# Optimization experiments

Hardware: AMD Instinct MI355X
Metric: run time of the kernel (lower is better)

## Reference

```python
import jax, jax.numpy as jnp
import numpy as np
import math

B = 65536
N_NUM = 64; N_CAT = 16; CAT_SIZE = 1000; EMB = 16
ND = 64; NA = 64; OUT = ND + NA; NSTEPS = 5; GAMMA = 1.5
NFEAT = N_NUM + N_CAT * EMB          # 320
NGROUPS = N_NUM + N_CAT              # 80
GROUP_IDX = np.repeat(np.arange(NGROUPS), [1] * N_NUM + [EMB] * N_CAT)  # len 320
RES_SCALE = math.sqrt(0.5)
BN_EPS = 1e-5


def setup_inputs() -> dict:
    keys = iter(jax.random.split(jax.random.key(0), 64))
    def rn(shape, std):
        return jax.random.normal(next(keys), shape, jnp.float32) * std
    def mk_bn(c, lead=()):
        # stacked (scale, bias, running_mean, running_var) along axis -2
        s = 1.0 + 0.05 * jax.random.normal(next(keys), (*lead, c), jnp.float32)
        b = 0.05 * jax.random.normal(next(keys), (*lead, c), jnp.float32)
        m = 0.05 * jax.random.normal(next(keys), (*lead, c), jnp.float32)
        v = 1.0 + 0.1 * jax.random.uniform(next(keys), (*lead, c), dtype=jnp.float32)
        return jnp.stack([s, b, m, v], axis=-2)
    inp = {}
    inp["x_num"] = jax.random.normal(next(keys), (B, N_NUM), jnp.float32)
    inp["x_cat"] = jax.random.randint(next(keys), (B, N_CAT), 0, CAT_SIZE)
    inp["emb_W"] = rn((N_CAT, CAT_SIZE, EMB), 0.1)
    inp["in_bn"] = mk_bn(NFEAT)
    inp["sh_W0"] = rn((NFEAT, 2 * OUT), 1.0 / math.sqrt(NFEAT))
    inp["sh_b0"] = jnp.zeros((2 * OUT,), jnp.float32)
    inp["sh_bn0"] = mk_bn(2 * OUT)
    inp["sh_W1"] = rn((OUT, 2 * OUT), 1.0 / math.sqrt(OUT))
    inp["sh_b1"] = jnp.zeros((2 * OUT,), jnp.float32)
    inp["sh_bn1"] = mk_bn(2 * OUT)
    inp["init_W"] = rn((2, OUT, 2 * OUT), 1.0 / math.sqrt(OUT))
    inp["init_b"] = jnp.zeros((2, 2 * OUT), jnp.float32)
    inp["init_bn"] = mk_bn(2 * OUT, (2,))
    inp["step_W"] = rn((NSTEPS, 2, OUT, 2 * OUT), 1.0 / math.sqrt(OUT))
    inp["step_b"] = jnp.zeros((NSTEPS, 2, 2 * OUT), jnp.float32)
    inp["step_bn"] = mk_bn(2 * OUT, (NSTEPS, 2))
    inp["att_W"] = rn((NSTEPS, NA, NGROUPS), 1.0 / math.sqrt(NA))
    inp["att_b"] = jnp.zeros((NSTEPS, NGROUPS), jnp.float32)
    inp["att_bn"] = mk_bn(NGROUPS, (NSTEPS,))
    inp["out_W"] = rn((ND, 1), 1.0 / math.sqrt(ND))
    inp["out_b"] = jnp.zeros((1,), jnp.float32)
    return inp


def bn_apply(x, p):
    s, b, m, v = p  # each [C]
    return (x - m) * jax.lax.rsqrt(v + BN_EPS) * s + b


def glu_layer(x, W, b, bn):
    h = bn_apply(x @ W + b, bn)          # [B, 2*OUT]
    o, g = jnp.split(h, 2, axis=1)
    return o * jax.nn.sigmoid(g)


def glu_block(x, W, b, bn):
    y = glu_layer(x, W, b, bn)
    return (x + y) * RES_SCALE if x.shape == y.shape else y


def sparsemax(z):
    # along axis=1; Martins & Astudillo 2016
    zs = -jnp.sort(-z, axis=1)
    cs = jnp.cumsum(zs, axis=1)
    r = jnp.arange(1, z.shape[1] + 1, dtype=z.dtype)
    support = (1.0 + r * zs) > cs
    k = jnp.maximum(support.sum(axis=1, keepdims=True), 1)
    cs_k = jnp.take_along_axis(cs, k - 1, axis=1)
    tau = (cs_k - 1.0) / k.astype(z.dtype)
    return jnp.maximum(z - tau, 0.0)


def _forward(x_num, x_cat, emb_W, in_bn, sh_W0, sh_b0, sh_bn0, sh_W1, sh_b1, sh_bn1,
             init_W, init_b, init_bn, step_W, step_b, step_bn, att_W, att_b, att_bn,
             out_W, out_b):
    # categorical embeddings: [B, N_CAT, EMB] -> [B, N_CAT*EMB]
    emb = emb_W[np.arange(N_CAT)[None, :], x_cat].reshape(x_cat.shape[0], -1)
    x = jnp.concatenate([x_num, emb], axis=1)  # [B, NFEAT]
    x = bn_apply(x, in_bn)

    def ft_shared(h):
        h = glu_block(h, sh_W0, sh_b0, sh_bn0)   # 320 -> 128, no residual
        return glu_block(h, sh_W1, sh_b1, sh_bn1)  # residual

    def ft_indep(h, W, b, bn):
        for i in range(W.shape[0]):
            h = glu_block(h, W[i], b[i], bn[i])
        return h

    out0 = ft_indep(ft_shared(x), init_W, init_b, init_bn)
    a = out0[:, ND:]
    prior = jnp.ones((x.shape[0], NGROUPS), x.dtype)
    decision_sum = jnp.zeros((x.shape[0], ND), x.dtype)
    for step in range(NSTEPS):
        logits = bn_apply(a @ att_W[step] + att_b[step], att_bn[step]) * prior
        mask_group = sparsemax(logits)           # [B, NGROUPS]
        prior = prior * (GAMMA - mask_group)
        mask = mask_group[:, GROUP_IDX]          # [B, NFEAT] (repeat_interleave)
        out = ft_indep(ft_shared(mask * x), step_W[step], step_b[step], step_bn[step])
        d, a = out[:, :ND], out[:, ND:]
        decision_sum = decision_sum + jax.nn.relu(d)
    return decision_sum @ out_W + out_b          # [B, 1]


def reference(x_num, x_cat, emb_W, in_bn, sh_W0, sh_b0, sh_bn0, sh_W1, sh_b1, sh_bn1,
              init_W, init_b, init_bn, step_W, step_b, step_bn, att_W, att_b, att_bn,
              out_W, out_b):
    return _forward(x_num, x_cat, emb_W, in_bn, sh_W0, sh_b0, sh_bn0, sh_W1, sh_b1,
                    sh_bn1, init_W, init_b, init_bn, step_W, step_b, step_bn,
                    att_W, att_b, att_bn, out_W, out_b)
```

## Files before the change

kernel.cpp:

```cpp
#include <hip/hip_runtime.h>
#include <math.h>
#include <stdint.h>

typedef _Float16 half_t;
typedef _Float16 half8 __attribute__((ext_vector_type(8)));
typedef __fp16 fp16x2 __attribute__((ext_vector_type(2)));
typedef float floatx4 __attribute__((ext_vector_type(4)));
typedef float floatx16 __attribute__((ext_vector_type(16)));

constexpr float BN_EPS_C = 1e-5f;
constexpr float RES_SCALE_C = 0.70710678118654752f;
constexpr float GAMMA_C = 1.5f;
#define B_TOT 65536

__device__ __forceinline__ uint32_t pack2(float y) {
    const half_t h = (half_t)y;
    const half_t l = (half_t)(y - (float)h);
    union { half_t f; unsigned short u; } a, b; a.f = h; b.f = l;
    return (uint32_t)a.u | ((uint32_t)b.u << 16);
}
__device__ __forceinline__ void unpack2(uint32_t v, half_t& h, half_t& l) {
    union { unsigned short u; half_t f; } a, b;
    a.u = (unsigned short)(v & 0xffffu); b.u = (unsigned short)(v >> 16);
    h = a.f; l = b.f;
}
__device__ __forceinline__ void split_pair(float y0, float y1, half_t& h0, half_t& l0, half_t& h1, half_t& l1) {
    fp16x2 hh = __builtin_amdgcn_cvt_pkrtz(y0, y1);
    fp16x2 ll = __builtin_amdgcn_cvt_pkrtz(y0 - (float)hh.x, y1 - (float)hh.y);
    h0 = (half_t)hh.x; l0 = (half_t)ll.x; h1 = (half_t)hh.y; l1 = (half_t)ll.y;
}
__device__ __forceinline__ void pack2_pair(float y0, float y1, uint32_t& w0, uint32_t& w1) {
    fp16x2 hh = __builtin_amdgcn_cvt_pkrtz(y0, y1);
    fp16x2 ll = __builtin_amdgcn_cvt_pkrtz(y0 - (float)hh.x, y1 - (float)hh.y);
    const uint32_t hb = __builtin_bit_cast(uint32_t, hh);
    const uint32_t lb = __builtin_bit_cast(uint32_t, ll);
    w0 = (hb & 0xffffu) | (lb << 16);
    w1 = (hb >> 16) | (lb & 0xffff0000u);
}
__device__ __forceinline__ void unpack8(const uint32_t* wv, half8& h, half8& l) {
#pragma unroll
    for (int j = 0; j < 8; ++j) {
        half_t hh, ll; unpack2(wv[j], hh, ll);
        h[j] = hh; l[j] = ll;
    }
}

__global__ void wsplit_kernel(const float* __restrict__ sh_W0, const float* __restrict__ sh_W1,
                              const float* __restrict__ init_W, const float* __restrict__ step_W,
                              half_t* __restrict__ Wh, half_t* __restrict__ Wl)
{
    const int b = blockIdx.x, n = threadIdx.x;
    const float* src; int k; size_t base;
    if (b < 320)      { src = sh_W0;           k = b;       base = 0; }
    else if (b < 448) { src = sh_W1;           k = b - 320; base = 81920; }
    else if (b < 576) { src = init_W;          k = b - 448; base = 114688; }
    else if (b < 704) { src = init_W + 32768;  k = b - 576; base = 147456; }
    else {
        int j = (b - 704) >> 7; k = (b - 704) & 127;
        src = step_W + (size_t)j * 32768; base = 180224 + (size_t)j * 32768;
    }
    float v = src[k * 256 + n];
    if (b >= 448) v *= RES_SCALE_C;
    const half_t hi = (half_t)v;
    const half_t lo = (half_t)(v - (float)hi);
    const size_t idx = base + (size_t)(((k >> 3) * 256 + n) * 8 + (k & 7));
    Wh[idx] = hi; Wl[idx] = lo;
}

__global__ void wsplit_att_kernel(const float* __restrict__ att_W,
                                  half_t* __restrict__ aWh, half_t* __restrict__ aWl)
{
    const int b = blockIdx.x;
    const int n = threadIdx.x;
    const int step = b >> 6, k = b & 63;
    const float v = att_W[(size_t)b * 80 + n] * RES_SCALE_C;
    const half_t h = (half_t)v;
    const half_t l = (half_t)(v - (float)h);
    const size_t idx = (size_t)step * 5120 + (size_t)(((k >> 3) * 80 + n) * 8 + (k & 7));
    aWh[idx] = h; aWl[idx] = l;
}

__global__ void embed_bn_kernel(const float* __restrict__ x_num, const int* __restrict__ x_cat,
                                const float* __restrict__ emb_W, const float* __restrict__ in_bn,
                                uint32_t* __restrict__ xp)
{
    const int idx = blockIdx.x * 256 + threadIdx.x;
    const int s = idx / 320, j = idx - s * 320;
    float v;
    if (j < 64) v = x_num[(size_t)s * 64 + j];
    else {
        const int c = (j - 64) >> 4, e = (j - 64) & 15;
        v = emb_W[(size_t)(c * 1000 + x_cat[(size_t)s * 16 + c]) * 16 + e];
    }
    const float val = (v - in_bn[640 + j]) * (in_bn[j] * __frsqrt_rn(in_bn[960 + j] + BN_EPS_C)) + in_bn[320 + j];
    xp[idx] = pack2(val);
}

__device__ __forceinline__ void bn_fold(const float* __restrict__ bn, const float* __restrict__ bias,
                                        int c, float& sc, float& sh)
{
    sc = bn[c] * __frsqrt_rn(bn[768 + c] + BN_EPS_C);
    sh = fmaf(bias[c] - bn[512 + c], sc, bn[256 + c]);
}

__device__ __forceinline__ float glu_val(float accO, float accG,
                                         float sc_o, float sh_o, float sc_g, float sh_g)
{
    const float o = fmaf(accO, sc_o, sh_o);
    const float g = fmaf(accG, sc_g, sh_g);
    const float e = __expf(-g);
    return o * __builtin_amdgcn_rcpf(1.f + e);
}

#define MFMA32(A, B, C) C = __builtin_amdgcn_mfma_f32_32x32x16_f16(A, B, C, 0, 0, 0)
#define MFMA16(A, B, C) C = __builtin_amdgcn_mfma_f32_16x16x32_f16(A, B, C, 0, 0, 0)

__device__ __forceinline__ void layer_accum(const half_t (*H_h)[136], const half_t (*H_l)[136],
                                            const half_t* __restrict__ Wh, const half_t* __restrict__ Wl,
                                            size_t off, int n32, int k8, int no, int m0, int rot,
                                            floatx16* accO, floatx16* accG)
{
#pragma unroll 2
    for (int s = 0; s < 8; ++s) {
        const int sl8 = (s + rot) & 7;
        const int kq = sl8 * 2 + k8;
        const size_t wo = off + (size_t)(kq * 256 + no + n32) * 8;
        const half8 bo_h = *(const half8*)(Wh + wo);
        const half8 bo_l = *(const half8*)(Wl + wo);
        const half8 bg_h = *(const half8*)(Wh + wo + 1024);
        const half8 bg_l = *(const half8*)(Wl + wo + 1024);
#pragma unroll
        for (int mt = 0; mt < 2; ++mt) {
            const half8 a_h = *(const half8*)&H_h[m0 + mt * 32 + n32][sl8 * 16 + k8 * 8];
            const half8 a_l = *(const half8*)&H_l[m0 + mt * 32 + n32][sl8 * 16 + k8 * 8];
            MFMA32(a_h, bo_h, accO[mt]); MFMA32(a_h, bg_h, accG[mt]);
            MFMA32(a_l, bo_h, accO[mt]); MFMA32(a_l, bg_h, accG[mt]);
            MFMA32(a_h, bo_l, accO[mt]); MFMA32(a_h, bg_l, accG[mt]);
        }
    }
}

template<bool MASK>
__global__ __launch_bounds__(512, 4)
void ft_chain(const uint32_t* __restrict__ xp, uint32_t* __restrict__ avp,
              const half_t* __restrict__ Wh, const half_t* __restrict__ Wl,
              const half_t* __restrict__ aWh, const half_t* __restrict__ aWl,
              const float* __restrict__ att_b, const float* __restrict__ att_bn,
              float* __restrict__ prior,
              const float* __restrict__ b1, const float* __restrict__ bn1,
              const float* __restrict__ b2, const float* __restrict__ bn2,
              const float* __restrict__ b3, const float* __restrict__ bn3,
              const float* __restrict__ b4, const float* __restrict__ bn4,
              size_t w3_off, size_t w4_off,
              float* __restrict__ ds, int wmode_last, int step)
{
    __shared__ __align__(16) char smem[79872];
    float    (*mgs)[84]  = (float    (*)[84])smem;
    uint32_t (*As0)[36]  = (uint32_t (*)[36])(smem + 43008);
    uint32_t (*As1)[36]  = (uint32_t (*)[36])(smem + 61440);
    half_t   (*H_h)[136] = (half_t   (*)[136])smem;
    half_t   (*H_l)[136] = (half_t   (*)[136])(smem + 34816);

    const int t = threadIdx.x;
    const int s0 = blockIdx.x * 128;
    const int w = t >> 6, lane = t & 63;
    const int wq = w & 3, wh = w >> 2;
    const int n32 = lane & 31, k8 = lane >> 5;
    const int quad = lane >> 4, l16 = lane & 15;
    const int no = 32 * wq;
    const int m0 = wh * 64;
    const int half_id = (blockIdx.x >> 8) & 1;
    const int rowA = t >> 2, kA8 = (t & 3) * 8;

    if (MASK) {
        floatx4 zacc[5];
#pragma unroll
        for (int nt = 0; nt < 5; ++nt) zacc[nt] = (floatx4){0.f, 0.f, 0.f, 0.f};
        const uint32_t* aprow = avp + (size_t)(s0 + w * 16 + l16) * 64 + quad * 8;
#pragma unroll
        for (int kc = 0; kc < 64; kc += 32) {
            uint32_t wv[8];
            *(uint4*)&wv[0] = *(const uint4*)(aprow + kc);
            *(uint4*)&wv[4] = *(const uint4*)(aprow + kc + 4);
            half8 a_h, a_l;
            unpack8(wv, a_h, a_l);
            const int kq = (kc >> 3) + quad;
#pragma unroll
            for (int nt = 0; nt < 5; ++nt) {
                const size_t wi = (size_t)(kq * 80 + nt * 16 + l16) * 8;
                const half8 b_h = *(const half8*)(aWh + wi);
                const half8 b_l = *(const half8*)(aWl + wi);
                MFMA16(a_h, b_h, zacc[nt]);
                MFMA16(a_l, b_h, zacc[nt]);
                MFMA16(a_h, b_l, zacc[nt]);
            }
        }
        float preg[5][4];
#pragma unroll
        for (int nt = 0; nt < 5; ++nt) {
            const int c = nt * 16 + l16;
            const float sc = att_bn[c] * __frsqrt_rn(att_bn[240 + c] + BN_EPS_C);
            const float sh = fmaf(att_b[c] - att_bn[160 + c], sc, att_bn[80 + c]);
#pragma unroll
            for (int r = 0; r < 4; ++r) {
                const int sl = w * 16 + quad * 4 + r;
                const float pr = (step == 0) ? 1.f : prior[(size_t)(s0 + sl) * 80 + c];
                preg[nt][r] = pr;
                mgs[sl][c] = fmaf(zacc[nt][r], sc, sh) * pr;
            }
        }
        __syncthreads();
        {
            const int samp = rowA, j0 = (t & 3) * 20;
            float zj[20], zmax = -1e30f;
#pragma unroll
            for (int j = 0; j < 20; ++j) { zj[j] = mgs[samp][j0 + j]; zmax = fmaxf(zmax, zj[j]); }
            zmax = fmaxf(zmax, __shfl_xor(zmax, 1));
            zmax = fmaxf(zmax, __shfl_xor(zmax, 2));
            float lo = zmax - 1.f, hi = zmax;
#pragma unroll 1
            for (int it = 0; it < 16; ++it) {
                const float mid = 0.5f * (lo + hi);
                float ssum = 0.f;
#pragma unroll
                for (int j = 0; j < 20; ++j) ssum += fmaxf(zj[j] - mid, 0.f);
                ssum += __shfl_xor(ssum, 1);
                ssum += __shfl_xor(ssum, 2);
                if (ssum >= 1.f) lo = mid; else hi = mid;
            }
            const float tau = 0.5f * (lo + hi);
#pragma unroll
            for (int j = 0; j < 20; ++j) mgs[samp][j0 + j] = fmaxf(zj[j] - tau, 0.f);
        }
        __syncthreads();
#pragma unroll
        for (int nt = 0; nt < 5; ++nt) {
            const int c = nt * 16 + l16;
#pragma unroll
            for (int r = 0; r < 4; ++r) {
                const int sl = w * 16 + quad * 4 + r;
                prior[(size_t)(s0 + sl) * 80 + c] = preg[nt][r] * (GAMMA_C - mgs[sl][c]);
            }
        }
    }

    floatx16 accO[2], accG[2];
#pragma unroll
    for (int i = 0; i < 2; ++i) { accO[i] = (floatx16)(0.f); accG[i] = (floatx16)(0.f); }

    const uint32_t* arow = xp + (size_t)(s0 + rowA) * 320 + kA8;
    uint32_t pfw[2][8];
    const int ic0 = half_id * 5;

    auto stage_half = [&](uint32_t (*Asb)[36], int c, int sl2, const uint32_t* pf) {
        const int kb = c * 32 + kA8 + sl2 * 4;
        uint4 out;
        if (MASK) {
            float m[4];
            if (c < 2) {
                const float4 mq = *(const float4*)&mgs[rowA][kb];
                m[0] = mq.x; m[1] = mq.y; m[2] = mq.z; m[3] = mq.w;
            } else {
                const float mg = mgs[rowA][64 + ((kb - 64) >> 4)];
                m[0] = m[1] = m[2] = m[3] = mg;
            }
            float y[4];
#pragma unroll
            for (int j = 0; j < 4; ++j) {
                half_t h, l; unpack2(pf[sl2 * 4 + j], h, l);
                y[j] = ((float)h + (float)l) * m[j];
            }
            uint32_t w0, w1, w2, w3;
            pack2_pair(y[0], y[1], w0, w1);
            pack2_pair(y[2], y[3], w2, w3);
            out = make_uint4(w0, w1, w2, w3);
        } else {
            out = *(const uint4*)&pf[sl2 * 4];
        }
        *(uint4*)&Asb[rowA][kA8 + sl2 * 4] = out;
    };

    {
        *(uint4*)&pfw[0][0] = *(const uint4*)(arow + ic0 * 32);
        *(uint4*)&pfw[0][4] = *(const uint4*)(arow + ic0 * 32 + 4);
        stage_half(As0, ic0, 0, pfw[0]);
        stage_half(As0, ic0, 1, pfw[0]);
        const int c1 = (ic0 + 1) % 10;
        *(uint4*)&pfw[1][0] = *(const uint4*)(arow + c1 * 32);
        *(uint4*)&pfw[1][4] = *(const uint4*)(arow + c1 * 32 + 4);
    }
    __syncthreads();

#pragma unroll
    for (int i = 0; i < 10; ++i) {
        const int cc = (ic0 + i) % 10;
        const int cn = (cc + 1 == 10) ? 0 : cc + 1;
        uint32_t (*AsC)[36] = (i & 1) ? As1 : As0;
        uint32_t (*AsN)[36] = (i & 1) ? As0 : As1;
        if (i <= 7) {
            const int c2 = (ic0 + i + 2) % 10;
            *(uint4*)&pfw[i & 1][0] = *(const uint4*)(arow + c2 * 32);
            *(uint4*)&pfw[i & 1][4] = *(const uint4*)(arow + c2 * 32 + 4);
        }
#pragma unroll
        for (int sl4 = 0; sl4 < 2; ++sl4) {
            if (i < 9) stage_half(AsN, cn, sl4, pfw[(i + 1) & 1]);
            const int kq = cc * 4 + sl4 * 2 + k8;
            const size_t wo = (size_t)(kq * 256 + no + n32) * 8;
            const half8 bo_h = *(const half8*)(Wh + wo);
            const half8 bo_l = *(const half8*)(Wl + wo);
            const half8 bg_h = *(const half8*)(Wh + wo + 1024);
            const half8 bg_l = *(const half8*)(Wl + wo + 1024);
#pragma unroll
            for (int mt = 0; mt < 2; ++mt) {
                uint32_t wv[8];
                *(uint4*)&wv[0] = *(const uint4*)&AsC[m0 + mt * 32 + n32][sl4 * 16 + k8 * 8];
                *(uint4*)&wv[4] = *(const uint4*)&AsC[m0 + mt * 32 + n32][sl4 * 16 + k8 * 8 + 4];
                half8 a_h, a_l;
                unpack8(wv, a_h, a_l);
                MFMA32(a_h, bo_h, accO[mt]); MFMA32(a_h, bg_h, accG[mt]);
                MFMA32(a_l, bo_h, accO[mt]); MFMA32(a_l, bg_h, accG[mt]);
                MFMA32(a_h, bo_l, accO[mt]); MFMA32(a_h, bg_l, accG[mt]);
            }
        }
        __syncthreads();
    }

    float yres[2][16];
    {
        const int c = no + n32;
        float sc_o, sh_o, sc_g, sh_g;
        bn_fold(bn1, b1, c, sc_o, sh_o);
        bn_fold(bn1, b1, c + 128, sc_g, sh_g);
#pragma unroll
        for (int mt = 0; mt < 2; ++mt)
#pragma unroll
            for (int q = 0; q < 4; ++q)
#pragma unroll
                for (int rp = 0; rp < 2; ++rp) {
                    const int r0 = q * 4 + rp * 2;
                    const int sl = m0 + mt * 32 + rp * 2 + 8 * q + 4 * k8;
                    const float y0 = glu_val(accO[mt][r0],     accG[mt][r0],     sc_o, sh_o, sc_g, sh_g);
                    const float y1 = glu_val(accO[mt][r0 + 1], accG[mt][r0 + 1], sc_o, sh_o, sc_g, sh_g);
                    yres[mt][r0] = y0; yres[mt][r0 + 1] = y1;
                    half_t h0, l0, h1, l1;
                    split_pair(y0, y1, h0, l0, h1, l1);
                    H_h[sl][c] = h0; H_l[sl][c] = l0;
                    H_h[sl + 1][c] = h1; H_l[sl + 1][c] = l1;
                }
    }
    __syncthreads();

#pragma unroll 1
    for (int layer = 0; layer < 2; ++layer) {
        const float* bb = layer ? b3 : b2;
        const float* bn = layer ? bn3 : bn2;
        const size_t off = layer ? w3_off : (size_t)81920;
        const float rs = layer ? RES_SCALE_C : 1.0f;
#pragma unroll
        for (int i = 0; i < 2; ++i) { accO[i] = (floatx16)(0.f); accG[i] = (floatx16)(0.f); }
        layer_accum(H_h, H_l, Wh, Wl, off, n32, k8, no, m0, half_id * 4, accO, accG);
        __syncthreads();
        {
            const int c = no + n32;
            float sc_o, sh_o, sc_g, sh_g;
            bn_fold(bn, bb, c, sc_o, sh_o);
            bn_fold(bn, bb, c + 128, sc_g, sh_g);
#pragma unroll
            for (int mt = 0; mt < 2; ++mt)
#pragma unroll
                for (int q = 0; q < 4; ++q)
#pragma unroll
                    for (int rp = 0; rp < 2; ++rp) {
                        const int r0 = q * 4 + rp * 2;
                        const int sl = m0 + mt * 32 + rp * 2 + 8 * q + 4 * k8;
                        const float y0 = fmaf(rs, yres[mt][r0],     glu_val(accO[mt][r0],     accG[mt][r0],     sc_o, sh_o, sc_g, sh_g));
                        const float y1 = fmaf(rs, yres[mt][r0 + 1], glu_val(accO[mt][r0 + 1], accG[mt][r0 + 1], sc_o, sh_o, sc_g, sh_g));
                        yres[mt][r0] = y0; yres[mt][r0 + 1] = y1;
                        half_t h0, l0, h1, l1;
                        split_pair(y0, y1, h0, l0, h1, l1);
                        H_h[sl][c] = h0; H_l[sl][c] = l0;
                        H_h[sl + 1][c] = h1; H_l[sl + 1][c] = l1;
                    }
        }
        __syncthreads();
    }

#pragma unroll
    for (int i = 0; i < 2; ++i) { accO[i] = (floatx16)(0.f); accG[i] = (floatx16)(0.f); }
    layer_accum(H_h, H_l, Wh, Wl, w4_off, n32, k8, no, m0, half_id * 4, accO, accG);
    {
        const int c = no + n32;
        float sc_o, sh_o, sc_g, sh_g;
        bn_fold(bn4, b4, c, sc_o, sh_o);
        bn_fold(bn4, b4, c + 128, sc_g, sh_g);
        if (wq < 2) {
            if (wmode_last != 1) {
#pragma unroll
                for (int mt = 0; mt < 2; ++mt)
#pragma unroll
                    for (int q = 0; q < 4; ++q)
#pragma unroll
                        for (int rp = 0; rp < 2; ++rp) {
                            const int r0 = q * 4 + rp * 2;
                            const int sl = m0 + mt * 32 + rp * 2 + 8 * q + 4 * k8;
                            const float y0 = fmaf(RES_SCALE_C, yres[mt][r0],     glu_val(accO[mt][r0],     accG[mt][r0],     sc_o, sh_o, sc_g, sh_g));
                            const float y1 = fmaf(RES_SCALE_C, yres[mt][r0 + 1], glu_val(accO[mt][r0 + 1], accG[mt][r0 + 1], sc_o, sh_o, sc_g, sh_g));
                            const float d0 = fmaxf(y0, 0.f);
                            const float d1 = fmaxf(y1, 0.f);
                            float* dp0 = ds + (size_t)(s0 + sl) * 64 + c;
                            float* dp1 = ds + (size_t)(s0 + sl + 1) * 64 + c;
                            if (wmode_last == 2) { *dp0 = d0; *dp1 = d1; }
                            else { *dp0 += d0; *dp1 += d1; }
                        }
            }
        } else {
#pragma unroll
            for (int mt = 0; mt < 2; ++mt)
#pragma unroll
                for (int q = 0; q < 4; ++q)
#pragma unroll
                    for (int rp = 0; rp < 2; ++rp) {
                        const int r0 = q * 4 + rp * 2;
                        const int sl = m0 + mt * 32 + rp * 2 + 8 * q + 4 * k8;
                        const float y0 = fmaf(RES_SCALE_C, yres[mt][r0],     glu_val(accO[mt][r0],     accG[mt][r0],     sc_o, sh_o, sc_g, sh_g));
                        const float y1 = fmaf(RES_SCALE_C, yres[mt][r0 + 1], glu_val(accO[mt][r0 + 1], accG[mt][r0 + 1], sc_o, sh_o, sc_g, sh_g));
                        uint32_t w0, w1;
                        pack2_pair(y0, y1, w0, w1);
                        avp[(size_t)(s0 + sl) * 64 + (c - 64)] = w0;
                        avp[(size_t)(s0 + sl + 1) * 64 + (c - 64)] = w1;
                    }
        }
    }
}

__global__ void final_kernel(const float* __restrict__ dsum, const float* __restrict__ out_W,
                             const float* __restrict__ out_b, float* __restrict__ out)
{
    const int s = blockIdx.x * 256 + threadIdx.x;
    float acc = 0.f;
    const float4* dp = (const float4*)(dsum + (size_t)s * 64);
    const float4* wp = (const float4*)out_W;
#pragma unroll
    for (int q = 0; q < 16; ++q) {
        const float4 d = dp[q];
        const float4 ww = wp[q];
        acc += d.x * ww.x + d.y * ww.y + d.z * ww.z + d.w * ww.w;
    }
    out[s] = fmaf(RES_SCALE_C, acc, out_b[0]);
}

extern "C" void kernel_launch(void* const* d_in, const int* in_sizes, int n_in,
                              void* d_out, int out_size, void* d_ws, size_t ws_size,
                              hipStream_t stream)
{
    const float* x_num  = (const float*)d_in[0];
    const int*   x_cat  = (const int*)d_in[1];
    const float* emb_W  = (const float*)d_in[2];
    const float* in_bn  = (const float*)d_in[3];
    const float* sh_W0  = (const float*)d_in[4];
    const float* sh_b0  = (const float*)d_in[5];
    const float* sh_bn0 = (const float*)d_in[6];
    const float* sh_W1  = (const float*)d_in[7];
    const float* sh_b1  = (const float*)d_in[8];
    const float* sh_bn1 = (const float*)d_in[9];
    const float* init_W = (const float*)d_in[10];
    const float* init_b = (const float*)d_in[11];
    const float* init_bn= (const float*)d_in[12];
    const float* step_W = (const float*)d_in[13];
    const float* step_b = (const float*)d_in[14];
    const float* step_bn= (const float*)d_in[15];
    const float* att_W  = (const float*)d_in[16];
    const float* att_b  = (const float*)d_in[17];
    const float* att_bn = (const float*)d_in[18];
    const float* out_W  = (const float*)d_in[19];
    const float* out_b  = (const float*)d_in[20];

    const size_t B = B_TOT;
    char* p = (char*)d_ws;
    uint32_t* xp  = (uint32_t*)p;  p += B * 320 * 4;
    uint32_t* avp = (uint32_t*)p;  p += B * 64 * 4;
    half_t* Wh    = (half_t*)p;    p += 507904 * 2;
    half_t* Wl    = (half_t*)p;    p += 507904 * 2;
    half_t* aWh   = (half_t*)p;    p += 25600 * 2;
    half_t* aWl   = (half_t*)p;    p += 25600 * 2;
    float* pri    = (float*)p;     p += B * 80 * 4;
    float* ds     = (float*)p;     p += B * 64 * 4;

    wsplit_kernel<<<1984, 256, 0, stream>>>(sh_W0, sh_W1, init_W, step_W, Wh, Wl);
    wsplit_att_kernel<<<320, 80, 0, stream>>>(att_W, aWh, aWl);
    embed_bn_kernel<<<(B_TOT * 320) / 256, 256, 0, stream>>>(x_num, x_cat, emb_W, in_bn, xp);

    const int GB = B_TOT / 128;
    ft_chain<false><<<GB, 512, 0, stream>>>(xp, avp, Wh, Wl,
                                            nullptr, nullptr, nullptr, nullptr, nullptr,
                                            sh_b0, sh_bn0, sh_b1, sh_bn1,
                                            init_b, init_bn, init_b + 256, init_bn + 1024,
                                            (size_t)114688, (size_t)147456, ds, 1, 0);
    for (int st = 0; st < 5; ++st) {
        const size_t w3 = 180224 + (size_t)(st * 2 + 0) * 32768;
        const size_t w4 = 180224 + (size_t)(st * 2 + 1) * 32768;
        ft_chain<true><<<GB, 512, 0, stream>>>(xp, avp, Wh, Wl,
                                               aWh + st * 5120, aWl + st * 5120,
                                               att_b + st * 80, att_bn + st * 320, pri,
                                               sh_b0, sh_bn0, sh_b1, sh_bn1,
                                               step_b + (st * 2 + 0) * 256, step_bn + (st * 2 + 0) * 1024,
                                               step_b + (st * 2 + 1) * 256, step_bn + (st * 2 + 1) * 1024,
                                               w3, w4, ds, st == 0 ? 2 : 3, st);
    }
    final_kernel<<<B_TOT / 256, 256, 0, stream>>>(ds, out_W, out_b, (float*)d_out);
}
```

Measured before the change: 688.9 us.

## Store split-fp16 input as separate hi/lo planes and prefold batchnorm params

Stores the split-precision input as two separate fp16 arrays instead of interleaved hi/lo words. The A tile is staged into separate hi/lo shared-memory buffers, which removes the per-MFMA unpack shuffling and lets the kernel read half8 vectors directly. BatchNorm scale and shift are folded once in a small kernel, so each ft_chain launch no longer recomputes rsqrt per channel. The shared-memory layout grows slightly, and the mgs row stride changes from 84 to 80 floats, which may add bank conflicts.

```diff
diff --git a/kernel.cpp b/kernel.cpp
--- a/kernel.cpp
+++ b/kernel.cpp
@@ -13,12 +13,6 @@
 constexpr float GAMMA_C = 1.5f;
 #define B_TOT 65536
 
-__device__ __forceinline__ uint32_t pack2(float y) {
-    const half_t h = (half_t)y;
-    const half_t l = (half_t)(y - (float)h);
-    union { half_t f; unsigned short u; } a, b; a.f = h; b.f = l;
-    return (uint32_t)a.u | ((uint32_t)b.u << 16);
-}
 __device__ __forceinline__ void unpack2(uint32_t v, half_t& h, half_t& l) {
     union { unsigned short u; half_t f; } a, b;
     a.u = (unsigned short)(v & 0xffffu); b.u = (unsigned short)(v >> 16);
@@ -80,9 +74,28 @@
     aWh[idx] = h; aWl[idx] = l;
 }
 
+__global__ void bnfold_kernel(const float* __restrict__ sh_bn0, const float* __restrict__ sh_b0,
+                              const float* __restrict__ sh_bn1, const float* __restrict__ sh_b1,
+                              const float* __restrict__ init_bn, const float* __restrict__ init_b,
+                              const float* __restrict__ step_bn, const float* __restrict__ step_b,
+                              float* __restrict__ bnf)
+{
+    const int layer = blockIdx.x, ch = threadIdx.x;
+    const float *bn, *bi;
+    if (layer == 0)      { bn = sh_bn0; bi = sh_b0; }
+    else if (layer == 1) { bn = sh_bn1; bi = sh_b1; }
+    else if (layer == 2) { bn = init_bn; bi = init_b; }
+    else if (layer == 3) { bn = init_bn + 1024; bi = init_b + 256; }
+    else                 { bn = step_bn + (layer - 4) * 1024; bi = step_b + (layer - 4) * 256; }
+    const float sc = bn[ch] * __frsqrt_rn(bn[768 + ch] + BN_EPS_C);
+    const float sh = fmaf(bi[ch] - bn[512 + ch], sc, bn[256 + ch]);
+    bnf[layer * 512 + ch] = sc;
+    bnf[layer * 512 + 256 + ch] = sh;
+}
+
 __global__ void embed_bn_kernel(const float* __restrict__ x_num, const int* __restrict__ x_cat,
                                 const float* __restrict__ emb_W, const float* __restrict__ in_bn,
-                                uint32_t* __restrict__ xp)
+                                half_t* __restrict__ xh, half_t* __restrict__ xl)
 {
     const int idx = blockIdx.x * 256 + threadIdx.x;
     const int s = idx / 320, j = idx - s * 320;
@@ -93,14 +106,9 @@
         v = emb_W[(size_t)(c * 1000 + x_cat[(size_t)s * 16 + c]) * 16 + e];
     }
     const float val = (v - in_bn[640 + j]) * (in_bn[j] * __frsqrt_rn(in_bn[960 + j] + BN_EPS_C)) + in_bn[320 + j];
-    xp[idx] = pack2(val);
-}
-
-__device__ __forceinline__ void bn_fold(const float* __restrict__ bn, const float* __restrict__ bias,
-                                        int c, float& sc, float& sh)
-{
-    sc = bn[c] * __frsqrt_rn(bn[768 + c] + BN_EPS_C);
-    sh = fmaf(bias[c] - bn[512 + c], sc, bn[256 + c]);
+    const half_t h = (half_t)val;
+    xh[idx] = h;
+    xl[idx] = (half_t)(val - (float)h);
 }
 
 __device__ __forceinline__ float glu_val(float accO, float accG,
@@ -142,24 +150,25 @@
 
 template<bool MASK>
 __global__ __launch_bounds__(512, 4)
-void ft_chain(const uint32_t* __restrict__ xp, uint32_t* __restrict__ avp,
+void ft_chain(const half_t* __restrict__ xh, const half_t* __restrict__ xl,
+              uint32_t* __restrict__ avp,
               const half_t* __restrict__ Wh, const half_t* __restrict__ Wl,
               const half_t* __restrict__ aWh, const half_t* __restrict__ aWl,
               const float* __restrict__ att_b, const float* __restrict__ att_bn,
               float* __restrict__ prior,
-              const float* __restrict__ b1, const float* __restrict__ bn1,
-              const float* __restrict__ b2, const float* __restrict__ bn2,
-              const float* __restrict__ b3, const float* __restrict__ bn3,
-              const float* __restrict__ b4, const float* __restrict__ bn4,
+              const float* __restrict__ bnf1, const float* __restrict__ bnf2,
+              const float* __restrict__ bnf3, const float* __restrict__ bnf4,
               size_t w3_off, size_t w4_off,
               float* __restrict__ ds, int wmode_last, int step)
 {
-    __shared__ __align__(16) char smem[79872];
-    float    (*mgs)[84]  = (float    (*)[84])smem;
-    uint32_t (*As0)[36]  = (uint32_t (*)[36])(smem + 43008);
-    uint32_t (*As1)[36]  = (uint32_t (*)[36])(smem + 61440);
-    half_t   (*H_h)[136] = (half_t   (*)[136])smem;
-    half_t   (*H_l)[136] = (half_t   (*)[136])(smem + 34816);
+    __shared__ __align__(16) char smem[81920];
+    float  (*mgs)[80]   = (float  (*)[80])smem;
+    half_t (*Ash0)[40]  = (half_t (*)[40])(smem + 40960);
+    half_t (*Asl0)[40]  = (half_t (*)[40])(smem + 51200);
+    half_t (*Ash1)[40]  = (half_t (*)[40])(smem + 61440);
+    half_t (*Asl1)[40]  = (half_t (*)[40])(smem + 71680);
+    half_t (*H_h)[136]  = (half_t (*)[136])smem;
+    half_t (*H_l)[136]  = (half_t (*)[136])(smem + 34816);
 
     const int t = threadIdx.x;
     const int s0 = blockIdx.x * 128;
@@ -248,46 +257,47 @@
 #pragma unroll
     for (int i = 0; i < 2; ++i) { accO[i] = (floatx16)(0.f); accG[i] = (floatx16)(0.f); }
 
-    const uint32_t* arow = xp + (size_t)(s0 + rowA) * 320 + kA8;
-    uint32_t pfw[2][8];
+    const half_t* xrh = xh + (size_t)(s0 + rowA) * 320 + kA8;
+    const half_t* xrl = xl + (size_t)(s0 + rowA) * 320 + kA8;
+    half8 pfh[2], pfl[2];
     const int ic0 = half_id * 5;
 
-    auto stage_half = [&](uint32_t (*Asb)[36], int c, int sl2, const uint32_t* pf) {
-        const int kb = c * 32 + kA8 + sl2 * 4;
-        uint4 out;
+    auto stage_chunk = [&](half_t (*Ah)[40], half_t (*Al)[40], int c, const half8& ph, const half8& pl) {
+        half8 hh, ll;
         if (MASK) {
-            float m[4];
+            const int kb = c * 32 + kA8;
+            float y[8];
             if (c < 2) {
-                const float4 mq = *(const float4*)&mgs[rowA][kb];
-                m[0] = mq.x; m[1] = mq.y; m[2] = mq.z; m[3] = mq.w;
+                const float4 m0q = *(const float4*)&mgs[rowA][kb];
+                const float4 m1q = *(const float4*)&mgs[rowA][kb + 4];
+                const float mm[8] = {m0q.x, m0q.y, m0q.z, m0q.w, m1q.x, m1q.y, m1q.z, m1q.w};
+#pragma unroll
+                for (int j = 0; j < 8; ++j) y[j] = ((float)ph[j] + (float)pl[j]) * mm[j];
             } else {
                 const float mg = mgs[rowA][64 + ((kb - 64) >> 4)];
-                m[0] = m[1] = m[2] = m[3] = mg;
-            }
-            float y[4];
-#pragma unroll
-            for (int j = 0; j < 4; ++j) {
-                half_t h, l; unpack2(pf[sl2 * 4 + j], h, l);
-                y[j] = ((float)h + (float)l) * m[j];
-            }
-            uint32_t w0, w1, w2, w3;
-            pack2_pair(y[0], y[1], w0, w1);
-            pack2_pair(y[2], y[3], w2, w3);
-            out = make_uint4(w0, w1, w2, w3);
+#pragma unroll
+                for (int j = 0; j < 8; ++j) y[j] = ((float)ph[j] + (float)pl[j]) * mg;
+            }
+#pragma unroll
+            for (int j = 0; j < 8; j += 2) {
+                half_t h0, l0, h1, l1;
+                split_pair(y[j], y[j + 1], h0, l0, h1, l1);
+                hh[j] = h0; hh[j + 1] = h1; ll[j] = l0; ll[j + 1] = l1;
+            }
         } else {
-            out = *(const uint4*)&pf[sl2 * 4];
-        }
-        *(uint4*)&Asb[rowA][kA8 + sl2 * 4] = out;
+            hh = ph; ll = pl;
+        }
+        *(half8*)&Ah[rowA][kA8] = hh;
+        *(half8*)&Al[rowA][kA8] = ll;
     };
 
     {
-        *(uint4*)&pfw[0][0] = *(const uint4*)(arow + ic0 * 32);
-        *(uint4*)&pfw[0][4] = *(const uint4*)(arow + ic0 * 32 + 4);
-        stage_half(As0, ic0, 0, pfw[0]);
-        stage_half(As0, ic0, 1, pfw[0]);
+        pfh[0] = *(const half8*)(xrh + ic0 * 32);
+        pfl[0] = *(const half8*)(xrl + ic0 * 32);
+        stage_chunk(Ash0, Asl0, ic0, pfh[0], pfl[0]);
         const int c1 = (ic0 + 1) % 10;
-        *(uint4*)&pfw[1][0] = *(const uint4*)(arow + c1 * 32);
-        *(uint4*)&pfw[1][4] = *(const uint4*)(arow + c1 * 32 + 4);
+        pfh[1] = *(const half8*)(xrh + c1 * 32);
+        pfl[1] = *(const half8*)(xrl + c1 * 32);
     }
     __syncthreads();
 
@@ -295,16 +305,18 @@
     for (int i = 0; i < 10; ++i) {
         const int cc = (ic0 + i) % 10;
         const int cn = (cc + 1 == 10) ? 0 : cc + 1;
-        uint32_t (*AsC)[36] = (i & 1) ? As1 : As0;
-        uint32_t (*AsN)[36] = (i & 1) ? As0 : As1;
+        half_t (*AhC)[40] = (i & 1) ? Ash1 : Ash0;
+        half_t (*AlC)[40] = (i & 1) ? Asl1 : Asl0;
+        half_t (*AhN)[40] = (i & 1) ? Ash0 : Ash1;
+        half_t (*AlN)[40] = (i & 1) ? Asl0 : Asl1;
         if (i <= 7) {
             const int c2 = (ic0 + i + 2) % 10;
-            *(uint4*)&pfw[i & 1][0] = *(const uint4*)(arow + c2 * 32);
-            *(uint4*)&pfw[i & 1][4] = *(const uint4*)(arow + c2 * 32 + 4);
-        }
+            pfh[i & 1] = *(const half8*)(xrh + c2 * 32);
+            pfl[i & 1] = *(const half8*)(xrl + c2 * 32);
+        }
+        if (i < 9) stage_chunk(AhN, AlN, cn, pfh[(i + 1) & 1], pfl[(i + 1) & 1]);
 #pragma unroll
         for (int sl4 = 0; sl4 < 2; ++sl4) {
-            if (i < 9) stage_half(AsN, cn, sl4, pfw[(i + 1) & 1]);
             const int kq = cc * 4 + sl4 * 2 + k8;
             const size_t wo = (size_t)(kq * 256 + no + n32) * 8;
             const half8 bo_h = *(const half8*)(Wh + wo);
@@ -313,11 +325,8 @@
             const half8 bg_l = *(const half8*)(Wl + wo + 1024);
 #pragma unroll
             for (int mt = 0; mt < 2; ++mt) {
-                uint32_t wv[8];
-                *(uint4*)&wv[0] = *(const uint4*)&AsC[m0 + mt * 32 + n32][sl4 * 16 + k8 * 8];
-                *(uint4*)&wv[4] = *(const uint4*)&AsC[m0 + mt * 32 + n32][sl4 * 16 + k8 * 8 + 4];
-                half8 a_h, a_l;
-                unpack8(wv, a_h, a_l);
+                const half8 a_h = *(const half8*)&AhC[m0 + mt * 32 + n32][sl4 * 16 + k8 * 8];
+                const half8 a_l = *(const half8*)&AlC[m0 + mt * 32 + n32][sl4 * 16 + k8 * 8];
                 MFMA32(a_h, bo_h, accO[mt]); MFMA32(a_h, bg_h, accG[mt]);
                 MFMA32(a_l, bo_h, accO[mt]); MFMA32(a_l, bg_h, accG[mt]);
                 MFMA32(a_h, bo_l, accO[mt]); MFMA32(a_h, bg_l, accG[mt]);
@@ -329,9 +338,8 @@
     float yres[2][16];
     {
         const int c = no + n32;
-        float sc_o, sh_o, sc_g, sh_g;
-        bn_fold(bn1, b1, c, sc_o, sh_o);
-        bn_fold(bn1, b1, c + 128, sc_g, sh_g);
+        const float sc_o = bnf1[c],       sh_o = bnf1[256 + c];
+        const float sc_g = bnf1[c + 128], sh_g = bnf1[384 + c];
 #pragma unroll
         for (int mt = 0; mt < 2; ++mt)
 #pragma unroll
@@ -353,8 +361,7 @@
 
 #pragma unroll 1
     for (int layer = 0; layer < 2; ++layer) {
-        const float* bb = layer ? b3 : b2;
-        const float* bn = layer ? bn3 : bn2;
+        const float* bf = layer ? bnf3 : bnf2;
         const size_t off = layer ? w3_off : (size_t)81920;
         const float rs = layer ? RES_SCALE_C : 1.0f;
 #pragma unroll
@@ -363,9 +370,8 @@
         __syncthreads();
         {
             const int c = no + n32;
-            float sc_o, sh_o, sc_g, sh_g;
-            bn_fold(bn, bb, c, sc_o, sh_o);
-            bn_fold(bn, bb, c + 128, sc_g, sh_g);
+            const float sc_o = bf[c],       sh_o = bf[256 + c];
+            const float sc_g = bf[c + 128], sh_g = bf[384 + c];
 #pragma unroll
             for (int mt = 0; mt < 2; ++mt)
 #pragma unroll
@@ -391,9 +397,8 @@
     layer_accum(H_h, H_l, Wh, Wl, w4_off, n32, k8, no, m0, half_id * 4, accO, accG);
     {
         const int c = no + n32;
-        float sc_o, sh_o, sc_g, sh_g;
-        bn_fold(bn4, b4, c, sc_o, sh_o);
-        bn_fold(bn4, b4, c + 128, sc_g, sh_g);
+        const float sc_o = bnf4[c],       sh_o = bnf4[256 + c];
+        const float sc_g = bnf4[c + 128], sh_g = bnf4[384 + c];
         if (wq < 2) {
             if (wmode_last != 1) {
 #pragma unroll
@@ -478,7 +483,8 @@
 
     const size_t B = B_TOT;
     char* p = (char*)d_ws;
-    uint32_t* xp  = (uint32_t*)p;  p += B * 320 * 4;
+    half_t* xh    = (half_t*)p;    p += B * 320 * 2;
+    half_t* xl    = (half_t*)p;    p += B * 320 * 2;
     uint32_t* avp = (uint32_t*)p;  p += B * 64 * 4;
     half_t* Wh    = (half_t*)p;    p += 507904 * 2;
     half_t* Wl    = (half_t*)p;    p += 507904 * 2;
@@ -486,26 +492,26 @@
     half_t* aWl   = (half_t*)p;    p += 25600 * 2;
     float* pri    = (float*)p;     p += B * 80 * 4;
     float* ds     = (float*)p;     p += B * 64 * 4;
+    float* bnf    = (float*)p;     p += 14 * 512 * 4;
 
     wsplit_kernel<<<1984, 256, 0, stream>>>(sh_W0, sh_W1, init_W, step_W, Wh, Wl);
     wsplit_att_kernel<<<320, 80, 0, stream>>>(att_W, aWh, aWl);
-    embed_bn_kernel<<<(B_TOT * 320) / 256, 256, 0, stream>>>(x_num, x_cat, emb_W, in_bn, xp);
+    bnfold_kernel<<<14, 256, 0, stream>>>(sh_bn0, sh_b0, sh_bn1, sh_b1, init_bn, init_b, step_bn, step_b, bnf);
+    embed_bn_kernel<<<(B_TOT * 320) / 256, 256, 0, stream>>>(x_num, x_cat, emb_W, in_bn, xh, xl);
 
     const int GB = B_TOT / 128;
-    ft_chain<false><<<GB, 512, 0, stream>>>(xp, avp, Wh, Wl,
+    ft_chain<false><<<GB, 512, 0, stream>>>(xh, xl, avp, Wh, Wl,
                                             nullptr, nullptr, nullptr, nullptr, nullptr,
-                                            sh_b0, sh_bn0, sh_b1, sh_bn1,
-                                            init_b, init_bn, init_b + 256, init_bn + 1024,
+                                            bnf, bnf + 512, bnf + 1024, bnf + 1536,
                                             (size_t)114688, (size_t)147456, ds, 1, 0);
     for (int st = 0; st < 5; ++st) {
         const size_t w3 = 180224 + (size_t)(st * 2 + 0) * 32768;
         const size_t w4 = 180224 + (size_t)(st * 2 + 1) * 32768;
-        ft_chain<true><<<GB, 512, 0, stream>>>(xp, avp, Wh, Wl,
+        ft_chain<true><<<GB, 512, 0, stream>>>(xh, xl, avp, Wh, Wl,
                                                aWh + st * 5120, aWl + st * 5120,
                                                att_b + st * 80, att_bn + st * 320, pri,
-                                               sh_b0, sh_bn0, sh_b1, sh_bn1,
-                                               step_b + (st * 2 + 0) * 256, step_bn + (st * 2 + 0) * 1024,
-                                               step_b + (st * 2 + 1) * 256, step_bn + (st * 2 + 1) * 1024,
+                                               bnf, bnf + 512,
+                                               bnf + (4 + 2 * st) * 512, bnf + (5 + 2 * st) * 512,
                                                w3, w4, ds, st == 0 ? 2 : 3, st);
     }
     final_kernel<<<B_TOT / 256, 256, 0, stream>>>(ds, out_W, out_b, (float*)d_out);
```

Measured after the change: 666.2 us (median of 2 runs). 3.3% less time.
